# Optimization experiments

Measured on AMD Instinct MI355X. Metric: run time of the kernel, lower is better.

Reference implementation:

```python
import jax, jax.numpy as jnp
import numpy as np

D = 192   # token_dim == channel_dim == expert_dim == adapt_dim (required by source code)
S = 4096  # sequence length
NE = 8    # num_experts


def _ln(x, g, b, eps=1e-5):
    m = x.mean(-1, keepdims=True)
    v = ((x - m) ** 2).mean(-1, keepdims=True)
    return (x - m) / jnp.sqrt(v + eps) * g + b


def _adaptive(x, a, W, b, AW, Ab):
    # AdaptiveLinear with adapt_method='add': weight = W + adapt(a).view(out, in)
    dW = (AW @ a + Ab).reshape(W.shape)
    return x @ (W + dW).T + b


def setup_inputs() -> dict:
    key = jax.random.key(0)
    ks = iter(jax.random.split(key, 40))

    def n(shape, s=0.05):
        return jax.random.normal(next(ks), shape, dtype=jnp.float32) * s

    return {
        "x": n((1, S, D), 1.0),
        "W_in": n((D, D)), "b_in": n((D,)),
        "feat_W": n((D, D)), "feat_b": n((D,)),
        "feat_AW": n((D * D, D)), "feat_Ab": n((D * D,)),
        "an_g": jnp.ones((D,)), "an_b": jnp.zeros((D,)),
        "tm_W": n((D, D)), "tm_b": n((D,)),
        "tm_AW": n((D * D, D)), "tm_Ab": n((D * D,)),
        "tn_g": jnp.ones((D,)), "tn_b": jnp.zeros((D,)),
        "cm_W": n((D, D)), "cm_b": n((D,)),
        "cm_AW": n((D * D, D)), "cm_Ab": n((D * D,)),
        "cn_g": jnp.ones((D,)), "cn_b": jnp.zeros((D,)),
        "pm_W": n((D, D)), "pm_b": n((D,)),
        "gate_W": n((NE, D)), "gate_b": n((NE,)),
        "ex_W": n((NE, D, D)), "ex_b": n((NE, D)),
        "ex_AW": n((NE, D * D, D)), "ex_Ab": n((NE, D * D)),
        "mn_g": jnp.ones((D,)), "mn_b": jnp.zeros((D,)),
        "out_W": n((D, D)), "out_b": n((D,)),
    }


def reference(x, W_in, b_in, feat_W, feat_b, feat_AW, feat_Ab, an_g, an_b,
              tm_W, tm_b, tm_AW, tm_Ab, tn_g, tn_b,
              cm_W, cm_b, cm_AW, cm_Ab, cn_g, cn_b,
              pm_W, pm_b, gate_W, gate_b, ex_W, ex_b, ex_AW, ex_Ab,
              mn_g, mn_b, out_W, out_b):
    h = x @ W_in.T + b_in                                        # [1,S,D]
    xm = h.mean(axis=1)                                          # [1,D]
    a = _adaptive(xm, xm[0], feat_W, feat_b, feat_AW, feat_Ab)   # [1,D]
    a = _ln(a, an_g, an_b)
    a0 = a[0]                                                    # [D]
    t = _adaptive(h, a0, tm_W, tm_b, tm_AW, tm_Ab)               # token mixing
    t = _ln(t, tn_g, tn_b)
    c = _adaptive(t, a0, cm_W, cm_b, cm_AW, cm_Ab)               # channel mixing
    c = _ln(c, cn_g, cn_b)
    m = c @ pm_W.T + pm_b                                        # pre-MoE [1,S,D]
    gate = jax.nn.softmax(a @ gate_W.T + gate_b, axis=-1)[0]     # [NE]
    # batched hypernet weight generation for all experts at once
    dW = (jnp.einsum('eka,a->ek', ex_AW, a0) + ex_Ab).reshape(NE, D, D)
    We = ex_W + dW                                               # [NE,D,D]
    ye = jnp.einsum('bsd,ned->nbse', m, We) + ex_b[:, None, None, :]
    eo = jnp.einsum('n,nbse->bse', gate, ye)                     # soft-MoE sum
    eo = _ln(eo, mn_g, mn_b)
    eo = jax.nn.relu(eo)
    return eo @ out_W.T + out_b
```

## Files before the change

kernel.cpp:

```cpp
#include <hip/hip_runtime.h>

#define DD 192
#define SROWS 16

__device__ __forceinline__ float dot192f(const float* __restrict__ row,
                                         const float* __restrict__ v) {
    const float4* p = (const float4*)row;
    float a0 = 0.f, a1 = 0.f, a2 = 0.f, a3 = 0.f;
#pragma unroll
    for (int c = 0; c < 48; c++) {
        float4 q = p[c];
        a0 = fmaf(q.x, v[4 * c + 0], a0);
        a1 = fmaf(q.y, v[4 * c + 1], a1);
        a2 = fmaf(q.z, v[4 * c + 2], a2);
        a3 = fmaf(q.w, v[4 * c + 3], a3);
    }
    return (a0 + a1) + (a2 + a3);
}

template <int POST, bool COLSUM>
__global__ __launch_bounds__(256) void stage_k(
    const float* __restrict__ A, const float* __restrict__ Wf,
    const float* __restrict__ bias, const float* __restrict__ g,
    const float* __restrict__ b, float* __restrict__ outF,
    float* __restrict__ colsum) {
    __shared__ float At[SROWS][196];
    __shared__ float WcT[32][193];
    const int tid = threadIdx.x;
    const int tr = tid >> 5, tc = tid & 31;
    const int r0 = blockIdx.x * SROWS;

    {
        const float4* Ap = (const float4*)(A + (size_t)r0 * DD);
        for (int e = tid; e < (SROWS * DD / 4); e += 256) {
            int r = e / 48, j4 = e % 48;
            float4 v = Ap[e];
            *(float4*)&At[r][j4 * 4] = v;
        }
    }
    float acc0[6], acc1[6];
#pragma unroll
    for (int ci = 0; ci < 6; ci++) {
        float bv = bias[ci * 32 + tc];
        acc0[ci] = bv;
        acc1[ci] = bv;
    }
    __syncthreads();

    const int ra = 2 * tr, rb = 2 * tr + 1;
    for (int jc = 0; jc < 6; jc++) {
        if (jc) __syncthreads();
        const int j0 = jc * 32;
        for (int e = tid; e < DD * 32; e += 256) {
            int i = e >> 5, jj = e & 31;
            WcT[jj][i] = Wf[i * DD + j0 + jj];
        }
        __syncthreads();
#pragma unroll
        for (int j = 0; j < 32; j++) {
            float a0v = At[ra][j0 + j];
            float a1v = At[rb][j0 + j];
#pragma unroll
            for (int ci = 0; ci < 6; ci++) {
                float w = WcT[j][ci * 32 + tc];
                acc0[ci] = fmaf(a0v, w, acc0[ci]);
                acc1[ci] = fmaf(a1v, w, acc1[ci]);
            }
        }
    }

    if (POST == 0) {
#pragma unroll
        for (int ci = 0; ci < 6; ci++) {
            int i = ci * 32 + tc;
            outF[(size_t)(r0 + ra) * DD + i] = acc0[ci];
            outF[(size_t)(r0 + rb) * DD + i] = acc1[ci];
        }
        if (COLSUM) {
            __syncthreads();
            float* cs = &WcT[0][0];
#pragma unroll
            for (int ci = 0; ci < 6; ci++)
                cs[tr * DD + ci * 32 + tc] = acc0[ci] + acc1[ci];
            __syncthreads();
            if (tid < DD) {
                float s = 0.f;
#pragma unroll
                for (int t = 0; t < 8; t++) s += cs[t * DD + tid];
                atomicAdd(&colsum[tid], s);
            }
        }
    } else {
        float s0 = 0, q0 = 0, s1 = 0, q1 = 0;
#pragma unroll
        for (int ci = 0; ci < 6; ci++) {
            s0 += acc0[ci]; q0 += acc0[ci] * acc0[ci];
            s1 += acc1[ci]; q1 += acc1[ci] * acc1[ci];
        }
#pragma unroll
        for (int m = 16; m >= 1; m >>= 1) {
            s0 += __shfl_xor(s0, m); q0 += __shfl_xor(q0, m);
            s1 += __shfl_xor(s1, m); q1 += __shfl_xor(q1, m);
        }
        const float inv = 1.f / 192.f;
        float m0 = s0 * inv, v0 = q0 * inv - m0 * m0;
        float m1 = s1 * inv, v1 = q1 * inv - m1 * m1;
        float rs0 = rsqrtf(v0 + 1e-5f), rs1 = rsqrtf(v1 + 1e-5f);
#pragma unroll
        for (int ci = 0; ci < 6; ci++) {
            int i = ci * 32 + tc;
            float gg = g[i], bb = b[i];
            float y0 = (acc0[ci] - m0) * rs0 * gg + bb;
            float y1 = (acc1[ci] - m1) * rs1 * gg + bb;
            if (POST == 2) { y0 = fmaxf(y0, 0.f); y1 = fmaxf(y1, 0.f); }
            outF[(size_t)(r0 + ra) * DD + i] = y0;
            outF[(size_t)(r0 + rb) * DD + i] = y1;
        }
    }
}

__global__ __launch_bounds__(256) void feat_k(
    const float* __restrict__ AW, const float* __restrict__ Ab,
    const float* __restrict__ Wm, const float* __restrict__ fb,
    const float* __restrict__ xm_sum, float* __restrict__ a_pre) {
    __shared__ float xm[DD];
    __shared__ float red[2];
    const int tid = threadIdx.x;
    if (tid < DD) xm[tid] = xm_sum[tid] * (1.f / 4096.f);
    if (tid < 2) red[tid] = 0.f;
    __syncthreads();
    int k = blockIdx.x * 256 + tid;
    int i = k / DD, j = k - i * DD;
    float val = dot192f(AW + (size_t)k * DD, xm) + Ab[k] + Wm[k];
    float contrib = xm[j] * val;
    if (j == 0) contrib += fb[i];
    int i0 = (blockIdx.x * 256) / DD;
    atomicAdd(&red[i - i0], contrib);
    __syncthreads();
    if (tid < 2) {
        int ii = i0 + tid;
        if (ii < DD) atomicAdd(&a_pre[ii], red[tid]);
    }
}

__global__ __launch_bounds__(192) void vec_k(
    const float* __restrict__ a_pre, const float* __restrict__ an_g,
    const float* __restrict__ an_b, const float* __restrict__ gate_W,
    const float* __restrict__ gate_b, const float* __restrict__ ex_b,
    float* __restrict__ a0g, float* __restrict__ gateg, float* __restrict__ b_moe) {
    __shared__ float a0s[DD];
    __shared__ float lg[8];
    __shared__ float red[6];
    const int t = threadIdx.x;
    float v = a_pre[t];
    float s = v, q = v * v;
#pragma unroll
    for (int m = 32; m >= 1; m >>= 1) {
        s += __shfl_xor(s, m);
        q += __shfl_xor(q, m);
    }
    if ((t & 63) == 0) { red[t >> 6] = s; red[3 + (t >> 6)] = q; }
    __syncthreads();
    float S = red[0] + red[1] + red[2];
    float Q = red[3] + red[4] + red[5];
    float mean = S / 192.f, var = Q / 192.f - mean * mean;
    float rs = rsqrtf(var + 1e-5f);
    float a0v = (v - mean) * rs * an_g[t] + an_b[t];
    a0s[t] = a0v;
    a0g[t] = a0v;
    __syncthreads();
    if (t < 8) {
        float acc = gate_b[t];
        for (int j = 0; j < DD; j++) acc = fmaf(a0s[j], gate_W[t * DD + j], acc);
        lg[t] = acc;
    }
    __syncthreads();
    if (t == 0) {
        float mx = lg[0];
        for (int e = 1; e < 8; e++) mx = fmaxf(mx, lg[e]);
        float sum = 0.f, ex[8];
        for (int e = 0; e < 8; e++) { ex[e] = expf(lg[e] - mx); sum += ex[e]; }
        for (int e = 0; e < 8; e++) lg[e] = ex[e] / sum;
    }
    __syncthreads();
    if (t < 8) gateg[t] = lg[t];
    float bm = 0.f;
#pragma unroll
    for (int e = 0; e < 8; e++) bm += lg[e] * ex_b[e * DD + t];
    b_moe[t] = bm;
}

__global__ __launch_bounds__(256) void build_k(
    const float* __restrict__ tm_W, const float* __restrict__ tm_AW,
    const float* __restrict__ tm_Ab, const float* __restrict__ cm_W,
    const float* __restrict__ cm_AW, const float* __restrict__ cm_Ab,
    const float* __restrict__ ex_W, const float* __restrict__ ex_AW,
    const float* __restrict__ ex_Ab, const float* __restrict__ a0g,
    const float* __restrict__ gateg, float* __restrict__ Wt, float* __restrict__ Wc,
    float* __restrict__ Wmoe) {
    __shared__ float a0[DD];
    const int t = threadIdx.x;
    if (t < DD) a0[t] = a0g[t];
    __syncthreads();
    const int b = blockIdx.x;
    if (b < 144) {
        int k = b * 256 + t;
        Wt[k] = tm_W[k] + dot192f(tm_AW + (size_t)k * DD, a0) + tm_Ab[k];
    } else if (b < 288) {
        int k = (b - 144) * 256 + t;
        Wc[k] = cm_W[k] + dot192f(cm_AW + (size_t)k * DD, a0) + cm_Ab[k];
    } else {
        int b2 = b - 288;
        int e = b2 / 144, c = b2 - e * 144;
        int k = c * 256 + t;
        size_t ek = (size_t)e * 36864 + k;
        float val = ex_W[ek] + dot192f(ex_AW + ek * DD, a0) + ex_Ab[ek];
        atomicAdd(&Wmoe[k], gateg[e] * val);
    }
}

extern "C" void kernel_launch(void* const* d_in, const int* in_sizes, int n_in,
                              void* d_out, int out_size, void* d_ws, size_t ws_size,
                              hipStream_t stream) {
    (void)in_sizes; (void)n_in; (void)out_size; (void)ws_size;
    const float* x       = (const float*)d_in[0];
    const float* W_in    = (const float*)d_in[1];
    const float* b_in    = (const float*)d_in[2];
    const float* feat_W  = (const float*)d_in[3];
    const float* feat_b  = (const float*)d_in[4];
    const float* feat_AW = (const float*)d_in[5];
    const float* feat_Ab = (const float*)d_in[6];
    const float* an_g    = (const float*)d_in[7];
    const float* an_b    = (const float*)d_in[8];
    const float* tm_W    = (const float*)d_in[9];
    const float* tm_b    = (const float*)d_in[10];
    const float* tm_AW   = (const float*)d_in[11];
    const float* tm_Ab   = (const float*)d_in[12];
    const float* tn_g    = (const float*)d_in[13];
    const float* tn_b    = (const float*)d_in[14];
    const float* cm_W    = (const float*)d_in[15];
    const float* cm_b    = (const float*)d_in[16];
    const float* cm_AW   = (const float*)d_in[17];
    const float* cm_Ab   = (const float*)d_in[18];
    const float* cn_g    = (const float*)d_in[19];
    const float* cn_b    = (const float*)d_in[20];
    const float* pm_W    = (const float*)d_in[21];
    const float* pm_b    = (const float*)d_in[22];
    const float* gate_W  = (const float*)d_in[23];
    const float* gate_b  = (const float*)d_in[24];
    const float* ex_W    = (const float*)d_in[25];
    const float* ex_b    = (const float*)d_in[26];
    const float* ex_AW   = (const float*)d_in[27];
    const float* ex_Ab   = (const float*)d_in[28];
    const float* mn_g    = (const float*)d_in[29];
    const float* mn_b    = (const float*)d_in[30];
    const float* out_W   = (const float*)d_in[31];
    const float* out_b   = (const float*)d_in[32];

    float* ws = (float*)d_ws;
    float* B0     = ws;
    float* B1     = ws + 786432;
    float* xm_sum = ws + 1572864;
    float* a_pre  = ws + 1573056;
    float* Wmoe   = ws + 1573248;
    float* Wt     = ws + 1610112;
    float* Wc     = ws + 1646976;
    float* a0     = ws + 1683840;
    float* gate   = ws + 1684032;
    float* b_moe  = ws + 1684040;

    hipMemsetAsync(xm_sum, 0, (size_t)(192 + 192 + 36864) * sizeof(float), stream);

    stage_k<0, true><<<256, 256, 0, stream>>>(x, W_in, b_in, nullptr, nullptr, B0, xm_sum);
    feat_k<<<144, 256, 0, stream>>>(feat_AW, feat_Ab, feat_W, feat_b, xm_sum, a_pre);
    vec_k<<<1, 192, 0, stream>>>(a_pre, an_g, an_b, gate_W, gate_b, ex_b, a0, gate, b_moe);
    build_k<<<1440, 256, 0, stream>>>(tm_W, tm_AW, tm_Ab, cm_W, cm_AW, cm_Ab, ex_W, ex_AW,
                                      ex_Ab, a0, gate, Wt, Wc, Wmoe);
    stage_k<1, false><<<256, 256, 0, stream>>>(B0, Wt, tm_b, tn_g, tn_b, B1, nullptr);
    stage_k<1, false><<<256, 256, 0, stream>>>(B1, Wc, cm_b, cn_g, cn_b, B0, nullptr);
    stage_k<0, false><<<256, 256, 0, stream>>>(B0, pm_W, pm_b, nullptr, nullptr, B1, nullptr);
    stage_k<2, false><<<256, 256, 0, stream>>>(B1, Wmoe, b_moe, mn_g, mn_b, B0, nullptr);
    stage_k<0, false><<<256, 256, 0, stream>>>(B0, out_W, out_b, nullptr, nullptr,
                                               (float*)d_out, nullptr);
}
```

Baseline: 593.4 us.

## Restructure hypernet weight build and row GEMMs with coalesced tiles and deferred LayerNorm

The hypernetwork dot products now stage 32 AW rows per block through shared memory with float4 loads, and 8 threads cooperate per row, replacing one strided row per thread. The row GEMM stages are split across three 64-column slices per 16-row block, giving more blocks, with a swizzled transposed weight tile. LayerNorm is deferred: each GEMM emits per-row sum and sum-of-squares via atomics, and the next stage applies normalization (and ReLU) while loading its input. This trades extra atomics and redundant A-tile loads per column slice for better memory coalescing and parallelism on the dominant AW streaming.

```diff
diff --git a/kernel.cpp b/kernel.cpp
--- a/kernel.cpp
+++ b/kernel.cpp
@@ -1,222 +1,273 @@
 #include <hip/hip_runtime.h>
 
 #define DD 192
-#define SROWS 16
-
-__device__ __forceinline__ float dot192f(const float* __restrict__ row,
-                                         const float* __restrict__ v) {
-    const float4* p = (const float4*)row;
-    float a0 = 0.f, a1 = 0.f, a2 = 0.f, a3 = 0.f;
-#pragma unroll
-    for (int c = 0; c < 48; c++) {
-        float4 q = p[c];
-        a0 = fmaf(q.x, v[4 * c + 0], a0);
-        a1 = fmaf(q.y, v[4 * c + 1], a1);
-        a2 = fmaf(q.z, v[4 * c + 2], a2);
-        a3 = fmaf(q.w, v[4 * c + 3], a3);
-    }
-    return (a0 + a1) + (a2 + a3);
-}
-
-template <int POST, bool COLSUM>
-__global__ __launch_bounds__(256) void stage_k(
-    const float* __restrict__ A, const float* __restrict__ Wf,
-    const float* __restrict__ bias, const float* __restrict__ g,
-    const float* __restrict__ b, float* __restrict__ outF,
-    float* __restrict__ colsum) {
-    __shared__ float At[SROWS][196];
-    __shared__ float WcT[32][193];
-    const int tid = threadIdx.x;
-    const int tr = tid >> 5, tc = tid & 31;
-    const int r0 = blockIdx.x * SROWS;
+
+template <int EMIT, int LNL>
+__global__ __launch_bounds__(256) void stage2_k(
+    const float* __restrict__ A, const float* __restrict__ W,
+    const float* __restrict__ bias,
+    const float* __restrict__ stats_in, const float* __restrict__ lng,
+    const float* __restrict__ lnb,
+    float* __restrict__ out, float* __restrict__ emit_buf) {
+    __shared__ float WT[DD * 64];
+    __shared__ float At[DD * 18];
+    __shared__ float ms[16], rs[16];
+    __shared__ float csum[4 * 64];
+
+    const int t = threadIdx.x;
+    const int tr = t >> 5, tc = t & 31;
+    const int b = blockIdx.x;
+    const int c0 = (b % 3) * 64;
+    const int r0 = (b / 3) * 16;
+
+    if (LNL > 0) {
+        if (t < 16) {
+            float s = stats_in[2 * (r0 + t)];
+            float q = stats_in[2 * (r0 + t) + 1];
+            float mean = s * (1.f / 192.f);
+            float var = q * (1.f / 192.f) - mean * mean;
+            ms[t] = mean;
+            rs[t] = rsqrtf(var + 1e-5f);
+        }
+        __syncthreads();
+    }
 
     {
-        const float4* Ap = (const float4*)(A + (size_t)r0 * DD);
-        for (int e = tid; e < (SROWS * DD / 4); e += 256) {
-            int r = e / 48, j4 = e % 48;
-            float4 v = Ap[e];
-            *(float4*)&At[r][j4 * 4] = v;
-        }
-    }
-    float acc0[6], acc1[6];
-#pragma unroll
-    for (int ci = 0; ci < 6; ci++) {
-        float bv = bias[ci * 32 + tc];
-        acc0[ci] = bv;
-        acc1[ci] = bv;
-    }
-    __syncthreads();
-
-    const int ra = 2 * tr, rb = 2 * tr + 1;
-    for (int jc = 0; jc < 6; jc++) {
-        if (jc) __syncthreads();
-        const int j0 = jc * 32;
-        for (int e = tid; e < DD * 32; e += 256) {
-            int i = e >> 5, jj = e & 31;
-            WcT[jj][i] = Wf[i * DD + j0 + jj];
-        }
-        __syncthreads();
-#pragma unroll
-        for (int j = 0; j < 32; j++) {
-            float a0v = At[ra][j0 + j];
-            float a1v = At[rb][j0 + j];
-#pragma unroll
-            for (int ci = 0; ci < 6; ci++) {
-                float w = WcT[j][ci * 32 + tc];
-                acc0[ci] = fmaf(a0v, w, acc0[ci]);
-                acc1[ci] = fmaf(a1v, w, acc1[ci]);
+        const float4* A4 = (const float4*)(A + (size_t)r0 * DD);
+#pragma unroll
+        for (int q = 0; q < 3; q++) {
+            int fidx = t + 256 * q;
+            int r = fidx / 48, jj = fidx - r * 48;
+            float4 v = A4[fidx];
+            if (LNL > 0) {
+                float mean = ms[r], rstd = rs[r];
+                float4 g4 = ((const float4*)lng)[jj];
+                float4 b4 = ((const float4*)lnb)[jj];
+                v.x = (v.x - mean) * rstd * g4.x + b4.x;
+                v.y = (v.y - mean) * rstd * g4.y + b4.y;
+                v.z = (v.z - mean) * rstd * g4.z + b4.z;
+                v.w = (v.w - mean) * rstd * g4.w + b4.w;
+                if (LNL == 2) {
+                    v.x = fmaxf(v.x, 0.f); v.y = fmaxf(v.y, 0.f);
+                    v.z = fmaxf(v.z, 0.f); v.w = fmaxf(v.w, 0.f);
+                }
             }
-        }
-    }
-
-    if (POST == 0) {
-#pragma unroll
-        for (int ci = 0; ci < 6; ci++) {
-            int i = ci * 32 + tc;
-            outF[(size_t)(r0 + ra) * DD + i] = acc0[ci];
-            outF[(size_t)(r0 + rb) * DD + i] = acc1[ci];
-        }
-        if (COLSUM) {
-            __syncthreads();
-            float* cs = &WcT[0][0];
-#pragma unroll
-            for (int ci = 0; ci < 6; ci++)
-                cs[tr * DD + ci * 32 + tc] = acc0[ci] + acc1[ci];
-            __syncthreads();
-            if (tid < DD) {
-                float s = 0.f;
-#pragma unroll
-                for (int t = 0; t < 8; t++) s += cs[t * DD + tid];
-                atomicAdd(&colsum[tid], s);
-            }
-        }
-    } else {
-        float s0 = 0, q0 = 0, s1 = 0, q1 = 0;
-#pragma unroll
-        for (int ci = 0; ci < 6; ci++) {
-            s0 += acc0[ci]; q0 += acc0[ci] * acc0[ci];
-            s1 += acc1[ci]; q1 += acc1[ci] * acc1[ci];
-        }
+            int j0 = 4 * jj;
+            At[(j0 + 0) * 18 + r] = v.x;
+            At[(j0 + 1) * 18 + r] = v.y;
+            At[(j0 + 2) * 18 + r] = v.z;
+            At[(j0 + 3) * 18 + r] = v.w;
+        }
+    }
+    {
+        const float4* W4 = (const float4*)(W + (size_t)c0 * DD);
+#pragma unroll
+        for (int q = 0; q < 12; q++) {
+            int fidx = t + 256 * q;
+            int ip = fidx / 48, jj = fidx - ip * 48;
+            float4 v = W4[fidx];
+            int j0 = 4 * jj;
+            WT[(j0 + 0) * 64 + ((ip + 2 * ((j0 + 0) & 31)) & 63)] = v.x;
+            WT[(j0 + 1) * 64 + ((ip + 2 * ((j0 + 1) & 31)) & 63)] = v.y;
+            WT[(j0 + 2) * 64 + ((ip + 2 * ((j0 + 2) & 31)) & 63)] = v.z;
+            WT[(j0 + 3) * 64 + ((ip + 2 * ((j0 + 3) & 31)) & 63)] = v.w;
+        }
+    }
+
+    const int i0 = c0 + 2 * tc;
+    float b0v = bias[i0], b1v = bias[i0 + 1];
+    float acc00 = b0v, acc01 = b1v, acc10 = b0v, acc11 = b1v;
+    __syncthreads();
+
+#pragma unroll 4
+    for (int j = 0; j < DD; j++) {
+        float2 a2 = *(const float2*)&At[j * 18 + 2 * tr];
+        int cs = (2 * tc + 2 * (j & 31)) & 63;
+        float2 w2 = *(const float2*)&WT[j * 64 + cs];
+        acc00 = fmaf(a2.x, w2.x, acc00);
+        acc01 = fmaf(a2.x, w2.y, acc01);
+        acc10 = fmaf(a2.y, w2.x, acc10);
+        acc11 = fmaf(a2.y, w2.y, acc11);
+    }
+
+    const int ra = r0 + 2 * tr, rb = ra + 1;
+    *(float2*)&out[(size_t)ra * DD + i0] = make_float2(acc00, acc01);
+    *(float2*)&out[(size_t)rb * DD + i0] = make_float2(acc10, acc11);
+
+    if (EMIT == 2) {
+        float s0 = acc00 + acc01, q0 = acc00 * acc00 + acc01 * acc01;
+        float s1 = acc10 + acc11, q1 = acc10 * acc10 + acc11 * acc11;
 #pragma unroll
         for (int m = 16; m >= 1; m >>= 1) {
             s0 += __shfl_xor(s0, m); q0 += __shfl_xor(q0, m);
             s1 += __shfl_xor(s1, m); q1 += __shfl_xor(q1, m);
         }
-        const float inv = 1.f / 192.f;
-        float m0 = s0 * inv, v0 = q0 * inv - m0 * m0;
-        float m1 = s1 * inv, v1 = q1 * inv - m1 * m1;
-        float rs0 = rsqrtf(v0 + 1e-5f), rs1 = rsqrtf(v1 + 1e-5f);
-#pragma unroll
-        for (int ci = 0; ci < 6; ci++) {
-            int i = ci * 32 + tc;
-            float gg = g[i], bb = b[i];
-            float y0 = (acc0[ci] - m0) * rs0 * gg + bb;
-            float y1 = (acc1[ci] - m1) * rs1 * gg + bb;
-            if (POST == 2) { y0 = fmaxf(y0, 0.f); y1 = fmaxf(y1, 0.f); }
-            outF[(size_t)(r0 + ra) * DD + i] = y0;
-            outF[(size_t)(r0 + rb) * DD + i] = y1;
-        }
-    }
-}
-
-__global__ __launch_bounds__(256) void feat_k(
-    const float* __restrict__ AW, const float* __restrict__ Ab,
-    const float* __restrict__ Wm, const float* __restrict__ fb,
-    const float* __restrict__ xm_sum, float* __restrict__ a_pre) {
-    __shared__ float xm[DD];
-    __shared__ float red[2];
-    const int tid = threadIdx.x;
-    if (tid < DD) xm[tid] = xm_sum[tid] * (1.f / 4096.f);
-    if (tid < 2) red[tid] = 0.f;
-    __syncthreads();
-    int k = blockIdx.x * 256 + tid;
-    int i = k / DD, j = k - i * DD;
-    float val = dot192f(AW + (size_t)k * DD, xm) + Ab[k] + Wm[k];
-    float contrib = xm[j] * val;
-    if (j == 0) contrib += fb[i];
-    int i0 = (blockIdx.x * 256) / DD;
-    atomicAdd(&red[i - i0], contrib);
-    __syncthreads();
-    if (tid < 2) {
-        int ii = i0 + tid;
-        if (ii < DD) atomicAdd(&a_pre[ii], red[tid]);
-    }
-}
-
-__global__ __launch_bounds__(192) void vec_k(
-    const float* __restrict__ a_pre, const float* __restrict__ an_g,
-    const float* __restrict__ an_b, const float* __restrict__ gate_W,
-    const float* __restrict__ gate_b, const float* __restrict__ ex_b,
-    float* __restrict__ a0g, float* __restrict__ gateg, float* __restrict__ b_moe) {
-    __shared__ float a0s[DD];
-    __shared__ float lg[8];
-    __shared__ float red[6];
-    const int t = threadIdx.x;
-    float v = a_pre[t];
-    float s = v, q = v * v;
-#pragma unroll
-    for (int m = 32; m >= 1; m >>= 1) {
-        s += __shfl_xor(s, m);
-        q += __shfl_xor(q, m);
-    }
-    if ((t & 63) == 0) { red[t >> 6] = s; red[3 + (t >> 6)] = q; }
-    __syncthreads();
-    float S = red[0] + red[1] + red[2];
-    float Q = red[3] + red[4] + red[5];
-    float mean = S / 192.f, var = Q / 192.f - mean * mean;
-    float rs = rsqrtf(var + 1e-5f);
-    float a0v = (v - mean) * rs * an_g[t] + an_b[t];
-    a0s[t] = a0v;
-    a0g[t] = a0v;
-    __syncthreads();
-    if (t < 8) {
-        float acc = gate_b[t];
-        for (int j = 0; j < DD; j++) acc = fmaf(a0s[j], gate_W[t * DD + j], acc);
-        lg[t] = acc;
-    }
-    __syncthreads();
-    if (t == 0) {
-        float mx = lg[0];
-        for (int e = 1; e < 8; e++) mx = fmaxf(mx, lg[e]);
-        float sum = 0.f, ex[8];
-        for (int e = 0; e < 8; e++) { ex[e] = expf(lg[e] - mx); sum += ex[e]; }
-        for (int e = 0; e < 8; e++) lg[e] = ex[e] / sum;
-    }
-    __syncthreads();
-    if (t < 8) gateg[t] = lg[t];
-    float bm = 0.f;
-#pragma unroll
-    for (int e = 0; e < 8; e++) bm += lg[e] * ex_b[e * DD + t];
-    b_moe[t] = bm;
-}
-
-__global__ __launch_bounds__(256) void build_k(
+        if (tc == 0) {
+            atomicAdd(&emit_buf[2 * ra], s0);
+            atomicAdd(&emit_buf[2 * ra + 1], q0);
+            atomicAdd(&emit_buf[2 * rb], s1);
+            atomicAdd(&emit_buf[2 * rb + 1], q1);
+        }
+    } else if (EMIT == 1) {
+        float cs0 = acc00 + acc10;
+        float cs1 = acc01 + acc11;
+        cs0 += __shfl_xor(cs0, 32);
+        cs1 += __shfl_xor(cs1, 32);
+        int w = t >> 6;
+        if ((t & 63) < 32) {
+            csum[w * 64 + 2 * tc] = cs0;
+            csum[w * 64 + 2 * tc + 1] = cs1;
+        }
+        __syncthreads();
+        if (t < 64) {
+            float s = csum[t] + csum[64 + t] + csum[128 + t] + csum[192 + t];
+            atomicAdd(&emit_buf[c0 + t], s);
+        }
+    }
+}
+
+__global__ __launch_bounds__(256) void hyper_k(
     const float* __restrict__ tm_W, const float* __restrict__ tm_AW,
     const float* __restrict__ tm_Ab, const float* __restrict__ cm_W,
     const float* __restrict__ cm_AW, const float* __restrict__ cm_Ab,
     const float* __restrict__ ex_W, const float* __restrict__ ex_AW,
     const float* __restrict__ ex_Ab, const float* __restrict__ a0g,
-    const float* __restrict__ gateg, float* __restrict__ Wt, float* __restrict__ Wc,
-    float* __restrict__ Wmoe) {
-    __shared__ float a0[DD];
+    const float* __restrict__ gateg, float* __restrict__ Wt,
+    float* __restrict__ Wc, float* __restrict__ Wmoe) {
+    __shared__ float a0s[DD];
+    __shared__ float rows[32 * 204];
+    __shared__ float wb[32], ab[32], vals[32];
     const int t = threadIdx.x;
-    if (t < DD) a0[t] = a0g[t];
-    __syncthreads();
     const int b = blockIdx.x;
-    if (b < 144) {
-        int k = b * 256 + t;
-        Wt[k] = tm_W[k] + dot192f(tm_AW + (size_t)k * DD, a0) + tm_Ab[k];
-    } else if (b < 288) {
-        int k = (b - 144) * 256 + t;
-        Wc[k] = cm_W[k] + dot192f(cm_AW + (size_t)k * DD, a0) + cm_Ab[k];
-    } else {
-        int b2 = b - 288;
-        int e = b2 / 144, c = b2 - e * 144;
-        int k = c * 256 + t;
-        size_t ek = (size_t)e * 36864 + k;
-        float val = ex_W[ek] + dot192f(ex_AW + ek * DD, a0) + ex_Ab[ek];
-        atomicAdd(&Wmoe[k], gateg[e] * val);
-    }
+    const float* AW; const float* WB; const float* AB;
+    int k0, mode, e = 0;
+    if (b < 1152)      { mode = 0; AW = tm_AW; WB = tm_W; AB = tm_Ab; k0 = b * 32; }
+    else if (b < 2304) { mode = 1; AW = cm_AW; WB = cm_W; AB = cm_Ab; k0 = (b - 1152) * 32; }
+    else {
+        mode = 2; int bb = b - 2304; e = bb / 1152; k0 = (bb - e * 1152) * 32;
+        AW = ex_AW + (size_t)e * 36864 * DD;
+        WB = ex_W + (size_t)e * 36864;
+        AB = ex_Ab + (size_t)e * 36864;
+    }
+    if (t < DD) a0s[t] = a0g[t];
+    if (t < 32) { wb[t] = WB[k0 + t]; ab[t] = AB[k0 + t]; }
+    const float4* src4 = (const float4*)(AW + (size_t)k0 * DD);
+#pragma unroll
+    for (int q = 0; q < 6; q++) {
+        int fidx = t + 256 * q;
+        int r = fidx / 48, jj = fidx - r * 48;
+        float4 v = src4[fidx];
+        *(float4*)&rows[r * 204 + 4 * jj] = v;
+    }
+    __syncthreads();
+    const int r = t >> 3, p = t & 7;
+    float acc = 0.f;
+#pragma unroll
+    for (int q = 0; q < 6; q++) {
+        int jo = p * 24 + 4 * q;
+        float4 w = *(const float4*)&rows[r * 204 + jo];
+        float4 aa = *(const float4*)&a0s[jo];
+        acc = fmaf(w.x, aa.x, acc); acc = fmaf(w.y, aa.y, acc);
+        acc = fmaf(w.z, aa.z, acc); acc = fmaf(w.w, aa.w, acc);
+    }
+    acc += __shfl_xor(acc, 1);
+    acc += __shfl_xor(acc, 2);
+    acc += __shfl_xor(acc, 4);
+    if (p == 0) vals[r] = acc + wb[r] + ab[r];
+    __syncthreads();
+    if (t < 32) {
+        if (mode == 0) Wt[k0 + t] = vals[t];
+        else if (mode == 1) Wc[k0 + t] = vals[t];
+        else atomicAdd(&Wmoe[k0 + t], gateg[e] * vals[t]);
+    }
+}
+
+__global__ __launch_bounds__(256) void feat2_k(
+    const float* __restrict__ feat_W, const float* __restrict__ feat_AW,
+    const float* __restrict__ feat_Ab, const float* __restrict__ xm_sum,
+    float* __restrict__ a_pre) {
+    __shared__ float xms[DD];
+    __shared__ float rows[32 * 204];
+    __shared__ float wb[32], ab[32], vals[32];
+    const int t = threadIdx.x;
+    const int k0 = blockIdx.x * 32;
+    if (t < DD) xms[t] = xm_sum[t] * (1.f / 4096.f);
+    if (t < 32) { wb[t] = feat_W[k0 + t]; ab[t] = feat_Ab[k0 + t]; }
+    const float4* src4 = (const float4*)(feat_AW + (size_t)k0 * DD);
+#pragma unroll
+    for (int q = 0; q < 6; q++) {
+        int fidx = t + 256 * q;
+        int r = fidx / 48, jj = fidx - r * 48;
+        float4 v = src4[fidx];
+        *(float4*)&rows[r * 204 + 4 * jj] = v;
+    }
+    __syncthreads();
+    const int r = t >> 3, p = t & 7;
+    float acc = 0.f;
+#pragma unroll
+    for (int q = 0; q < 6; q++) {
+        int jo = p * 24 + 4 * q;
+        float4 w = *(const float4*)&rows[r * 204 + jo];
+        float4 aa = *(const float4*)&xms[jo];
+        acc = fmaf(w.x, aa.x, acc); acc = fmaf(w.y, aa.y, acc);
+        acc = fmaf(w.z, aa.z, acc); acc = fmaf(w.w, aa.w, acc);
+    }
+    acc += __shfl_xor(acc, 1);
+    acc += __shfl_xor(acc, 2);
+    acc += __shfl_xor(acc, 4);
+    if (p == 0) vals[r] = acc + wb[r] + ab[r];
+    __syncthreads();
+    const int j0 = k0 % DD;
+    if (t < 32) {
+        float c = vals[t] * xms[j0 + t];
+#pragma unroll
+        for (int m = 16; m >= 1; m >>= 1) c += __shfl_xor(c, m);
+        if (t == 0) atomicAdd(&a_pre[k0 / DD], c);
+    }
+}
+
+__global__ __launch_bounds__(192) void vec_k(
+    const float* __restrict__ a_pre, const float* __restrict__ feat_b,
+    const float* __restrict__ an_g, const float* __restrict__ an_b,
+    const float* __restrict__ gate_W, const float* __restrict__ gate_b,
+    const float* __restrict__ ex_b, float* __restrict__ a0g,
+    float* __restrict__ gateg, float* __restrict__ b_moe) {
+    __shared__ float lgs[8];
+    __shared__ float red[6];
+    const int t = threadIdx.x;
+    float v = a_pre[t] + feat_b[t];
+    float s = v, q = v * v;
+#pragma unroll
+    for (int m = 32; m >= 1; m >>= 1) {
+        s += __shfl_xor(s, m);
+        q += __shfl_xor(q, m);
+    }
+    if ((t & 63) == 0) { red[t >> 6] = s; red[3 + (t >> 6)] = q; }
+    if (t < 8) lgs[t] = gate_b[t];
+    __syncthreads();
+    float S = red[0] + red[1] + red[2];
+    float Q = red[3] + red[4] + red[5];
+    float mean = S * (1.f / 192.f);
+    float var = Q * (1.f / 192.f) - mean * mean;
+    float rstd = rsqrtf(var + 1e-5f);
+    float a0v = (v - mean) * rstd * an_g[t] + an_b[t];
+    a0g[t] = a0v;
+#pragma unroll
+    for (int e = 0; e < 8; e++) atomicAdd(&lgs[e], a0v * gate_W[e * DD + t]);
+    __syncthreads();
+    if (t == 0) {
+        float mx = lgs[0];
+        for (int e = 1; e < 8; e++) mx = fmaxf(mx, lgs[e]);
+        float sum = 0.f, ex[8];
+        for (int e = 0; e < 8; e++) { ex[e] = expf(lgs[e] - mx); sum += ex[e]; }
+        for (int e = 0; e < 8; e++) lgs[e] = ex[e] / sum;
+    }
+    __syncthreads();
+    if (t < 8) gateg[t] = lgs[t];
+    float bm = 0.f;
+#pragma unroll
+    for (int e = 0; e < 8; e++) bm = fmaf(lgs[e], ex_b[e * DD + t], bm);
+    b_moe[t] = bm;
 }
 
 extern "C" void kernel_launch(void* const* d_in, const int* in_sizes, int n_in,
@@ -262,24 +313,31 @@
     float* B1     = ws + 786432;
     float* xm_sum = ws + 1572864;
     float* a_pre  = ws + 1573056;
-    float* Wmoe   = ws + 1573248;
-    float* Wt     = ws + 1610112;
-    float* Wc     = ws + 1646976;
-    float* a0     = ws + 1683840;
-    float* gate   = ws + 1684032;
-    float* b_moe  = ws + 1684040;
-
-    hipMemsetAsync(xm_sum, 0, (size_t)(192 + 192 + 36864) * sizeof(float), stream);
-
-    stage_k<0, true><<<256, 256, 0, stream>>>(x, W_in, b_in, nullptr, nullptr, B0, xm_sum);
-    feat_k<<<144, 256, 0, stream>>>(feat_AW, feat_Ab, feat_W, feat_b, xm_sum, a_pre);
-    vec_k<<<1, 192, 0, stream>>>(a_pre, an_g, an_b, gate_W, gate_b, ex_b, a0, gate, b_moe);
-    build_k<<<1440, 256, 0, stream>>>(tm_W, tm_AW, tm_Ab, cm_W, cm_AW, cm_Ab, ex_W, ex_AW,
-                                      ex_Ab, a0, gate, Wt, Wc, Wmoe);
-    stage_k<1, false><<<256, 256, 0, stream>>>(B0, Wt, tm_b, tn_g, tn_b, B1, nullptr);
-    stage_k<1, false><<<256, 256, 0, stream>>>(B1, Wc, cm_b, cn_g, cn_b, B0, nullptr);
-    stage_k<0, false><<<256, 256, 0, stream>>>(B0, pm_W, pm_b, nullptr, nullptr, B1, nullptr);
-    stage_k<2, false><<<256, 256, 0, stream>>>(B1, Wmoe, b_moe, mn_g, mn_b, B0, nullptr);
-    stage_k<0, false><<<256, 256, 0, stream>>>(B0, out_W, out_b, nullptr, nullptr,
-                                               (float*)d_out, nullptr);
-}
+    float* st1    = ws + 1573248;
+    float* st2    = ws + 1581440;
+    float* st3    = ws + 1589632;
+    float* Wmoe   = ws + 1597824;
+    float* Wt     = ws + 1634688;
+    float* Wc     = ws + 1671552;
+    float* a0     = ws + 1708416;
+    float* gate   = ws + 1708608;
+    float* b_moe  = ws + 1708616;
+
+    hipMemsetAsync(xm_sum, 0, (size_t)61824 * sizeof(float), stream);
+
+    stage2_k<1, 0><<<768, 256, 0, stream>>>(x, W_in, b_in, nullptr, nullptr, nullptr,
+                                            B0, xm_sum);
+    feat2_k<<<1152, 256, 0, stream>>>(feat_W, feat_AW, feat_Ab, xm_sum, a_pre);
+    vec_k<<<1, 192, 0, stream>>>(a_pre, feat_b, an_g, an_b, gate_W, gate_b, ex_b,
+                                 a0, gate, b_moe);
+    hyper_k<<<11520, 256, 0, stream>>>(tm_W, tm_AW, tm_Ab, cm_W, cm_AW, cm_Ab,
+                                       ex_W, ex_AW, ex_Ab, a0, gate, Wt, Wc, Wmoe);
+    stage2_k<2, 0><<<768, 256, 0, stream>>>(B0, Wt, tm_b, nullptr, nullptr, nullptr,
+                                            B1, st1);
+    stage2_k<2, 1><<<768, 256, 0, stream>>>(B1, Wc, cm_b, st1, tn_g, tn_b, B0, st2);
+    stage2_k<0, 1><<<768, 256, 0, stream>>>(B0, pm_W, pm_b, st2, cn_g, cn_b, B1, nullptr);
+    stage2_k<2, 0><<<768, 256, 0, stream>>>(B1, Wmoe, b_moe, nullptr, nullptr, nullptr,
+                                            B0, st3);
+    stage2_k<0, 2><<<768, 256, 0, stream>>>(B0, out_W, out_b, st3, mn_g, mn_b,
+                                            (float*)d_out, nullptr);
+}
```

After: 566.9 us. 1.05x faster.
